# Performance work log

Measured on AMD Instinct MI355X. Metric: run time of the kernel, lower is better.

Reference implementation:

```python
import jax, jax.numpy as jnp
import numpy as np

GAMMA = 0.3      # LinearSpike surrogate slope (Bellec et al. 2018)
TIMESTEPS = 8
DROPOUT = 0.2

@jax.custom_vjp
def spike_fn(mem_thr):
    # forward: Heaviside spike; backward: piecewise-linear surrogate
    return (mem_thr > 0).astype(mem_thr.dtype)

def _spike_fwd(m):
    return (m > 0).astype(m.dtype), m

def _spike_bwd(m, g):
    return (GAMMA * jnp.maximum(1.0 - jnp.abs(m), 0.0) * g,)

spike_fn.defvjp(_spike_fwd, _spike_bwd)

def conv(x, w, stride=1, pad=1):
    return jax.lax.conv_general_dilated(
        x, w, (stride, stride), [(pad, pad), (pad, pad)],
        dimension_numbers=('NCHW', 'OIHW', 'NCHW'))

def avgpool2(x):
    B, C, H, W = x.shape
    return x.reshape(B, C, H // 2, 2, W // 2, 2).mean(axis=(3, 5))

def lif(mem, delta, leak, thr):
    mem = leak * mem + delta                  # leaky integrate
    mem_thr = mem / thr - 1.0                 # normalized membrane
    out = spike_fn(mem_thr)                   # binary spike
    mem = mem - thr * (mem_thr > 0).astype(mem.dtype)  # soft reset
    return mem, out

def setup_inputs() -> dict:
    key = jax.random.key(0)
    ks = jax.random.split(key, 24)
    B = 32
    def w(k, o, i, kh):
        std = float(np.sqrt(2.0 / (kh * kh * o)))  # matches _initialize_weights2
        return jax.random.normal(k, (o, i, kh, kh), jnp.float32) * std
    def mask(k, shape):
        keep = jax.random.bernoulli(k, 1.0 - DROPOUT, shape)
        return keep.astype(jnp.float32) / (1.0 - DROPOUT)
    return {
        'x': jax.random.normal(ks[0], (B, 3, 32, 32), jnp.float32),
        'w_pre0': w(ks[1], 64, 3, 3),
        'w_pre1': w(ks[2], 64, 64, 3),
        'w_pre2': w(ks[3], 64, 64, 3),
        'w1a': w(ks[4], 64, 64, 3),  'w1b': w(ks[5], 64, 64, 3),
        'w2a': w(ks[6], 128, 64, 3), 'w2b': w(ks[7], 128, 128, 3), 'w2i': w(ks[8], 128, 64, 1),
        'w3a': w(ks[9], 256, 128, 3), 'w3b': w(ks[10], 256, 256, 3), 'w3i': w(ks[11], 256, 128, 1),
        'w4a': w(ks[12], 512, 256, 3), 'w4b': w(ks[13], 512, 512, 3), 'w4i': w(ks[14], 512, 256, 1),
        'w_fc': jax.random.normal(ks[15], (10, 512 * 2 * 2), jnp.float32) * 0.01,
        'thr': jnp.ones((11,), jnp.float32),
        'leak': jnp.ones((11,), jnp.float32),
        'mask2': mask(ks[16], (B, 64, 32, 32)),
        'mask5': mask(ks[17], (B, 64, 32, 32)),
        'mask9': mask(ks[18], (B, 64, 16, 16)),
        'mask11': mask(ks[19], (B, 128, 8, 8)),
        'mask13': mask(ks[20], (B, 256, 4, 4)),
        'mask15': mask(ks[21], (B, 512, 2, 2)),
    }

def _forward(x, w_pre0, w_pre1, w_pre2, w1a, w1b, w2a, w2b, w2i,
             w3a, w3b, w3i, w4a, w4b, w4i, w_fc, thr, leak,
             mask2, mask5, mask9, mask11, mask13, mask15):
    B = x.shape[0]
    f32 = jnp.float32
    mems0 = (
        jnp.zeros((B, 64, 32, 32), f32), jnp.zeros((B, 64, 32, 32), f32),
        jnp.zeros((B, 64, 32, 32), f32),
        jnp.zeros((B, 64, 16, 16), f32), jnp.zeros((B, 64, 16, 16), f32),
        jnp.zeros((B, 128, 8, 8), f32), jnp.zeros((B, 128, 8, 8), f32),
        jnp.zeros((B, 256, 4, 4), f32), jnp.zeros((B, 256, 4, 4), f32),
        jnp.zeros((B, 512, 2, 2), f32), jnp.zeros((B, 512, 2, 2), f32),
        jnp.zeros((B, 10), f32),  # output accumulator mem
    )

    def step(carry, _):
        m0, m1, m2, m3, m4, m5, m6, m7, m8, m9, m10, mfc = carry
        # pre_process: (conv->spike->dropout) x2, conv->spike, avgpool2
        m0, o = lif(m0, conv(x, w_pre0), leak[0], thr[0]); o = o * mask2
        m1, o = lif(m1, conv(o, w_pre1), leak[1], thr[1]); o = o * mask5
        m2, o = lif(m2, conv(o, w_pre2), leak[2], thr[2])
        o = avgpool2(o)  # 32x32 -> 16x16
        # layer1 BasicBlock (stride 1, identity shortcut)
        inp = o
        m3, o = lif(m3, conv(inp, w1a), leak[3], thr[3]); o = o * mask9
        m4, o = lif(m4, conv(o, w1b) + inp, leak[4], thr[4])
        # layer2 BasicBlock (stride 2, 1x1 conv shortcut)
        inp = o
        m5, o = lif(m5, conv(inp, w2a, stride=2), leak[5], thr[5]); o = o * mask11
        m6, o = lif(m6, conv(o, w2b) + conv(inp, w2i, stride=2, pad=0), leak[6], thr[6])
        # layer3
        inp = o
        m7, o = lif(m7, conv(inp, w3a, stride=2), leak[7], thr[7]); o = o * mask13
        m8, o = lif(m8, conv(o, w3b) + conv(inp, w3i, stride=2, pad=0), leak[8], thr[8])
        # layer4
        inp = o
        m9, o = lif(m9, conv(inp, w4a, stride=2), leak[9], thr[9]); o = o * mask15
        m10, o = lif(m10, conv(o, w4b) + conv(inp, w4i, stride=2, pad=0), leak[10], thr[10])
        # output layer: pure accumulation of classifier current over timesteps
        mfc = mfc + o.reshape(B, -1) @ w_fc.T
        return (m0, m1, m2, m3, m4, m5, m6, m7, m8, m9, m10, mfc), None

    carry, _ = jax.lax.scan(step, mems0, None, length=TIMESTEPS)
    return carry[-1]  # [B, labels]

def reference(x, w_pre0, w_pre1, w_pre2, w1a, w1b, w2a, w2b, w2i,
              w3a, w3b, w3i, w4a, w4b, w4i, w_fc, thr, leak,
              mask2, mask5, mask9, mask11, mask13, mask15):
    return _forward(x, w_pre0, w_pre1, w_pre2, w1a, w1b, w2a, w2b, w2i,
                    w3a, w3b, w3i, w4a, w4b, w4i, w_fc, thr, leak,
                    mask2, mask5, mask9, mask11, mask13, mask15)
```

## Files before the change

kernel.cpp:

```cpp
#include <hip/hip_runtime.h>

#define BATCH 32

__device__ __forceinline__ float4 ld4(const float* p) { return *(const float4*)p; }

template<int H, int KS>
__global__ __launch_bounds__(256) void conv64_v2(
    const float* __restrict__ in, const float* __restrict__ w,
    float* __restrict__ pbuf)
{
    constexpr int W    = H;
    constexpr int QR   = W / 4;
    constexpr int ROWS = 64 / QR;
    constexpr int RS   = W + 4;
    constexpr int CCT  = 64 / KS;
    constexpr int CC   = (CCT < 8) ? CCT : 8;
    constexpr int NCH  = CCT / CC;
    constexpr int PLANE = (ROWS + 2) * RS;
    constexpr int NTOT = 32 * 64 * H * W;
    constexpr int LCNT = CC * (ROWS + 2) * (W + 2);
    static_assert(NCH == 1 || NCH == 2, "pipeline supports <=2 chunks");
    __shared__ float sIn[CC * PLANE];

    const int tid  = threadIdx.x;
    const int b    = blockIdx.x;
    const int rt   = blockIdx.y;
    const int zc   = blockIdx.z;
    const int cg   = zc & 1;
    const int ks   = zc >> 1;
    const int lane = tid & 63;
    const int g    = __builtin_amdgcn_readfirstlane(tid >> 6);
    const int octet = cg * 32 + g * 8;
    const int r    = lane / QR;
    const int wq   = lane % QR;
    const int ho   = rt * ROWS + r;
    const int row0 = rt * ROWS;

    float acc[8][4] = {};
    const size_t in_b = (size_t)b * 64 * H * W;

    auto stage_val = [&](int i, int c0, float& v) -> int {
        int c   = i / ((ROWS + 2) * (W + 2));
        int rr  = (i / (W + 2)) % (ROWS + 2);
        int col = i % (W + 2);
        int ih  = row0 + rr - 1;
        int iw  = col - 1;
        v = 0.f;
        if ((unsigned)ih < (unsigned)H && (unsigned)iw < (unsigned)W)
            v = in[in_b + (size_t)(c0 + c) * H * W + ih * W + iw];
        return c * PLANE + rr * RS + col;
    };

    auto compute_chunk = [&](int c0) {
        for (int c = 0; c < CC; ++c) {
            float rv[3][6];
            #pragma unroll
            for (int dr = 0; dr < 3; ++dr) {
                const float* p = &sIn[c * PLANE + (r + dr) * RS + wq * 4];
                float4 a  = ld4(p);
                float2 b2 = *(const float2*)(p + 4);
                rv[dr][0] = a.x;  rv[dr][1] = a.y; rv[dr][2] = a.z; rv[dr][3] = a.w;
                rv[dr][4] = b2.x; rv[dr][5] = b2.y;
            }
            const float* wc = w + ((size_t)octet * 64 + (c0 + c)) * 9;
            #pragma unroll
            for (int j = 0; j < 8; ++j) {
                const float* wk = wc + (size_t)j * 64 * 9;
                float w0 = wk[0], w1 = wk[1], w2 = wk[2];
                float w3 = wk[3], w4 = wk[4], w5 = wk[5];
                float w6 = wk[6], w7 = wk[7], w8 = wk[8];
                #pragma unroll
                for (int k = 0; k < 4; ++k) {
                    acc[j][k] = fmaf(rv[0][k + 0], w0, acc[j][k]);
                    acc[j][k] = fmaf(rv[0][k + 1], w1, acc[j][k]);
                    acc[j][k] = fmaf(rv[0][k + 2], w2, acc[j][k]);
                    acc[j][k] = fmaf(rv[1][k + 0], w3, acc[j][k]);
                    acc[j][k] = fmaf(rv[1][k + 1], w4, acc[j][k]);
                    acc[j][k] = fmaf(rv[1][k + 2], w5, acc[j][k]);
                    acc[j][k] = fmaf(rv[2][k + 0], w6, acc[j][k]);
                    acc[j][k] = fmaf(rv[2][k + 1], w7, acc[j][k]);
                    acc[j][k] = fmaf(rv[2][k + 2], w8, acc[j][k]);
                }
            }
        }
    };

    if constexpr (NCH == 1) {
        for (int i = tid; i < LCNT; i += 256) {
            float v; int o = stage_val(i, ks * CCT, v); sIn[o] = v;
        }
        __syncthreads();
        compute_chunk(ks * CCT);
    } else {
        for (int i = tid; i < LCNT; i += 256) {
            float v; int o = stage_val(i, ks * CCT, v); sIn[o] = v;
        }
        constexpr int PF = (LCNT + 255) / 256;
        float pf[PF]; int po[PF];
        #pragma unroll
        for (int k = 0; k < PF; ++k) {
            int i = tid + k * 256; pf[k] = 0.f; po[k] = -1;
            if (i < LCNT) po[k] = stage_val(i, ks * CCT + CC, pf[k]);
        }
        __syncthreads();
        compute_chunk(ks * CCT);
        __syncthreads();
        #pragma unroll
        for (int k = 0; k < PF; ++k) if (po[k] >= 0) sIn[po[k]] = pf[k];
        __syncthreads();
        compute_chunk(ks * CCT + CC);
    }

    #pragma unroll
    for (int j = 0; j < 8; ++j) {
        const size_t idx = ((size_t)(b * 64 + octet + j) * H + ho) * W + wq * 4;
        *(float4*)&pbuf[(size_t)ks * NTOT + idx] =
            make_float4(acc[j][0], acc[j][1], acc[j][2], acc[j][3]);
    }
}

template<int CI, int CO, int KS, int RT>
__global__ __launch_bounds__(256) void conv_mid(
    const float* __restrict__ in, const float* __restrict__ w,
    float* __restrict__ pbuf)
{
    constexpr int HIN = 16, HOUT = 8;
    constexpr int CC  = CI / KS;
    constexpr int NR  = (RT - 1) * 2 + 3;
    constexpr int BSTR = NR * HIN + 4;
    constexpr int CST  = 32 * BSTR;
    constexpr int NTOT = 32 * CO * HOUT * HOUT;
    __shared__ float sBuf[CC * CST];

    const int tid  = threadIdx.x;
    const int lane = tid & 63;
    const int b    = lane >> 1;
    const int ks   = blockIdx.x;
    const int co_u = __builtin_amdgcn_readfirstlane(blockIdx.y * 4 + (tid >> 6));
    const int r0   = blockIdx.z * RT;
    const int g0   = r0 * 2 - 1;

    for (int i = tid; i < CC * 32 * NR * 4; i += 256) {
        int q  = i % 4;
        int s  = (i / 4) % NR;
        int bb = (i / (4 * NR)) % 32;
        int c  = i / (4 * NR * 32);
        int gr = g0 + s;
        float4 v = make_float4(0.f, 0.f, 0.f, 0.f);
        if ((unsigned)gr < (unsigned)HIN)
            v = ld4(&in[(((size_t)bb * CI + ks * CC + c) * HIN + gr) * HIN + q * 4]);
        *(float4*)&sBuf[c * CST + bb * BSTR + s * HIN + q * 4] = v;
    }
    __syncthreads();

    float acc[RT * 8] = {};
    #pragma unroll
    for (int c = 0; c < CC; ++c) {
        const float* wk = w + ((size_t)co_u * CI + ks * CC + c) * 9;
        float wr[9];
        #pragma unroll
        for (int q = 0; q < 9; ++q) wr[q] = wk[q];
        float pl[NR * HIN];
        #pragma unroll
        for (int k = 0; k < NR * 4; ++k) {
            float4 v = ld4(&sBuf[c * CST + b * BSTR + k * 4]);
            pl[k * 4 + 0] = v.x; pl[k * 4 + 1] = v.y;
            pl[k * 4 + 2] = v.z; pl[k * 4 + 3] = v.w;
        }
        #pragma unroll
        for (int j = 0; j < RT; ++j) {
            #pragma unroll
            for (int ow = 0; ow < 8; ++ow) {
                #pragma unroll
                for (int kh = 0; kh < 3; ++kh) {
                    const int s = 2 * j + kh;
                    #pragma unroll
                    for (int kw = 0; kw < 3; ++kw) {
                        const int iw = 2 * ow - 1 + kw;
                        if (iw < 0 || iw >= HIN) continue;
                        acc[j * 8 + ow] = fmaf(pl[s * HIN + iw], wr[kh * 3 + kw],
                                               acc[j * 8 + ow]);
                    }
                }
            }
        }
    }

    if ((lane & 1) == 0) {
        #pragma unroll
        for (int j = 0; j < RT; ++j) {
            const size_t idx = ((size_t)(b * CO + co_u) * HOUT + r0 + j) * HOUT;
            *(float4*)&pbuf[(size_t)ks * NTOT + idx] =
                make_float4(acc[j * 8 + 0], acc[j * 8 + 1], acc[j * 8 + 2], acc[j * 8 + 3]);
            *(float4*)&pbuf[(size_t)ks * NTOT + idx + 4] =
                make_float4(acc[j * 8 + 4], acc[j * 8 + 5], acc[j * 8 + 6], acc[j * 8 + 7]);
        }
    }
}

template<int KS>
__global__ __launch_bounds__(256) void conv_l2b(
    const float* __restrict__ in,
    const float* __restrict__ w,
    const float* __restrict__ sc_in,
    const float* __restrict__ sc_w,
    float* __restrict__ pbuf)
{
    constexpr int CI = 128, CO = 128, SC_CI = 64;
    constexpr int CC  = CI / KS;
    constexpr int SCC = SC_CI / KS;
    constexpr int BSTR = 52, CST = 32 * BSTR;
    constexpr int BSTRs = 36, CSTs = 32 * BSTRs;
    constexpr int NTOT = 32 * CO * 64;
    __shared__ float sBuf[CC * CST];

    const int tid  = threadIdx.x;
    const int lane = tid & 63;
    const int b    = lane >> 1;
    const int co_u = __builtin_amdgcn_readfirstlane(blockIdx.y * 4 + (tid >> 6));
    const int ks   = blockIdx.x;
    const int r0   = blockIdx.z * 4;

    for (int i = tid; i < CC * 32 * 12; i += 256) {
        int f4  = i % 2;
        int row = (i / 2) % 6;
        int bb  = (i / 12) % 32;
        int c   = i / 384;
        int gr  = r0 - 1 + row;
        float4 v = make_float4(0.f, 0.f, 0.f, 0.f);
        if ((unsigned)gr < 8u)
            v = ld4(&in[(((size_t)bb * CI + ks * CC + c) * 8 + gr) * 8 + f4 * 4]);
        *(float4*)&sBuf[c * CST + bb * BSTR + row * 8 + f4 * 4] = v;
    }
    __syncthreads();

    float acc[32] = {};
    #pragma unroll 2
    for (int c = 0; c < CC; ++c) {
        const float* wk = w + ((size_t)co_u * CI + ks * CC + c) * 9;
        float wr[9];
        #pragma unroll
        for (int q = 0; q < 9; ++q) wr[q] = wk[q];
        float pl[48];
        #pragma unroll
        for (int k = 0; k < 12; ++k) {
            float4 v = ld4(&sBuf[c * CST + b * BSTR + k * 4]);
            pl[k * 4 + 0] = v.x; pl[k * 4 + 1] = v.y;
            pl[k * 4 + 2] = v.z; pl[k * 4 + 3] = v.w;
        }
        #pragma unroll
        for (int oh = 0; oh < 4; ++oh) {
            #pragma unroll
            for (int ow = 0; ow < 8; ++ow) {
                #pragma unroll
                for (int kh = 0; kh < 3; ++kh) {
                    #pragma unroll
                    for (int kw = 0; kw < 3; ++kw) {
                        const int iw = ow - 1 + kw;
                        if (iw < 0 || iw >= 8) continue;
                        acc[oh * 8 + ow] = fmaf(pl[(oh + kh) * 8 + iw],
                                                wr[kh * 3 + kw], acc[oh * 8 + ow]);
                    }
                }
            }
        }
    }
    __syncthreads();

    for (int i = tid; i < SCC * 32 * 16; i += 256) {
        int q   = i % 4;
        int row = (i / 4) % 4;
        int bb  = (i / 16) % 32;
        int c   = i / 512;
        float4 v = ld4(&sc_in[
            (((size_t)bb * SC_CI + ks * SCC + c) * 16 + 2 * (r0 + row)) * 16 + q * 4]);
        sBuf[c * CSTs + bb * BSTRs + row * 8 + q * 2 + 0] = v.x;
        sBuf[c * CSTs + bb * BSTRs + row * 8 + q * 2 + 1] = v.z;
    }
    __syncthreads();

    #pragma unroll
    for (int c = 0; c < SCC; ++c) {
        float sw = sc_w[(size_t)co_u * SC_CI + ks * SCC + c];
        #pragma unroll
        for (int p4 = 0; p4 < 8; ++p4) {
            float4 v = ld4(&sBuf[c * CSTs + b * BSTRs + p4 * 4]);
            acc[p4 * 4 + 0] = fmaf(v.x, sw, acc[p4 * 4 + 0]);
            acc[p4 * 4 + 1] = fmaf(v.y, sw, acc[p4 * 4 + 1]);
            acc[p4 * 4 + 2] = fmaf(v.z, sw, acc[p4 * 4 + 2]);
            acc[p4 * 4 + 3] = fmaf(v.w, sw, acc[p4 * 4 + 3]);
        }
    }

    if ((lane & 1) == 0) {
        #pragma unroll
        for (int oh = 0; oh < 4; ++oh) {
            const size_t idx = ((size_t)(b * CO + co_u) * 8 + r0 + oh) * 8;
            *(float4*)&pbuf[(size_t)ks * NTOT + idx]     =
                make_float4(acc[oh * 8 + 0], acc[oh * 8 + 1], acc[oh * 8 + 2], acc[oh * 8 + 3]);
            *(float4*)&pbuf[(size_t)ks * NTOT + idx + 4] =
                make_float4(acc[oh * 8 + 4], acc[oh * 8 + 5], acc[oh * 8 + 6], acc[oh * 8 + 7]);
        }
    }
}

template<int CI, int HIN, int STRIDE, int CO, int SC_CI, int SC_HIN,
         int KS, int COB>
__global__ __launch_bounds__(COB * 64) void conv_ks(
    const float* __restrict__ in, const float* __restrict__ w,
    const float* __restrict__ sc_in, const float* __restrict__ sc_w,
    float* __restrict__ pbuf)
{
    constexpr int NT   = COB * 64;
    constexpr int HOUT = (STRIDE == 2) ? HIN / 2 : HIN;
    constexpr int P    = HOUT * HOUT;
    constexpr int NPIX = HIN * HIN;
    constexpr int CC   = CI / KS;
    constexpr int SCC  = (SC_CI > 0) ? SC_CI / KS : 0;
    constexpr int BSTR = NPIX + (((NPIX / 4) % 2 == 0) ? 4 : 0);
    constexpr int CST  = 32 * BSTR;
    constexpr int BSTRs = P + (((P / 4) % 2 == 0) ? 4 : 0);
    constexpr int CSTs  = 32 * BSTRs;
    static_assert(CI % KS == 0, "ks split");
    static_assert(NPIX % 4 == 0 && P % 4 == 0, "vector widths");

    __shared__ float sIn[CC * CST];
    __shared__ float sSc[(SCC > 0) ? SCC * CSTs : 1];

    const int tid  = threadIdx.x;
    const int lane = tid & 63;
    const int b    = lane >> 1;
    const int ks   = blockIdx.x;
    const int co_u = __builtin_amdgcn_readfirstlane(blockIdx.y * COB + (tid >> 6));
    const int cb   = ks * CC;

    constexpr int NF4 = CC * 32 * (NPIX / 4);
    for (int i = tid; i < NF4; i += NT) {
        int k4 = i % (NPIX / 4);
        int c  = (i / (NPIX / 4)) % CC;
        int bb = i / ((NPIX / 4) * CC);
        float4 v = ld4(&in[((size_t)bb * CI + cb + c) * NPIX + k4 * 4]);
        *(float4*)&sIn[c * CST + bb * BSTR + k4 * 4] = v;
    }
    if constexpr (SCC > 0) {
        constexpr int NH  = HOUT / 2;
        constexpr int NSC = SCC * 32 * HOUT * NH;
        for (int i = tid; i < NSC; i += NT) {
            int hc = i % NH;
            int r  = (i / NH) % HOUT;
            int c  = (i / (NH * HOUT)) % SCC;
            int bb = i / (NH * HOUT * SCC);
            float4 v = ld4(&sc_in[
                ((size_t)(bb * SC_CI + ks * SCC + c) * SC_HIN + 2 * r) * SC_HIN
                + hc * 4]);
            sSc[c * CSTs + bb * BSTRs + r * HOUT + hc * 2 + 0] = v.x;
            sSc[c * CSTs + bb * BSTRs + r * HOUT + hc * 2 + 1] = v.z;
        }
    }
    __syncthreads();

    float acc[P] = {};

    const float* wbase = w + ((size_t)co_u * CI + cb) * 9;
    #pragma unroll 4
    for (int j = 0; j < CC; ++j) {
        float wr[9];
        #pragma unroll
        for (int q = 0; q < 9; ++q) wr[q] = wbase[j * 9 + q];
        float plane[NPIX];
        #pragma unroll
        for (int r4 = 0; r4 < NPIX / 4; ++r4) {
            float4 v = ld4(&sIn[j * CST + b * BSTR + r4 * 4]);
            plane[r4 * 4 + 0] = v.x; plane[r4 * 4 + 1] = v.y;
            plane[r4 * 4 + 2] = v.z; plane[r4 * 4 + 3] = v.w;
        }
        #pragma unroll
        for (int ho = 0; ho < HOUT; ++ho) {
            #pragma unroll
            for (int wo = 0; wo < HOUT; ++wo) {
                #pragma unroll
                for (int kh = 0; kh < 3; ++kh) {
                    const int ih = ho * STRIDE - 1 + kh;
                    if (ih < 0 || ih >= HIN) continue;
                    #pragma unroll
                    for (int kw = 0; kw < 3; ++kw) {
                        const int iw = wo * STRIDE - 1 + kw;
                        if (iw < 0 || iw >= HIN) continue;
                        acc[ho * HOUT + wo] =
                            fmaf(plane[ih * HIN + iw], wr[kh * 3 + kw],
                                 acc[ho * HOUT + wo]);
                    }
                }
            }
        }
    }

    if constexpr (SCC > 0) {
        const float* swb = sc_w + (size_t)co_u * SC_CI + ks * SCC;
        #pragma unroll 4
        for (int j = 0; j < SCC; ++j) {
            float sw = swb[j];
            #pragma unroll
            for (int p4 = 0; p4 < P / 4; ++p4) {
                float4 v = ld4(&sSc[j * CSTs + b * BSTRs + p4 * 4]);
                acc[p4 * 4 + 0] = fmaf(v.x, sw, acc[p4 * 4 + 0]);
                acc[p4 * 4 + 1] = fmaf(v.y, sw, acc[p4 * 4 + 1]);
                acc[p4 * 4 + 2] = fmaf(v.z, sw, acc[p4 * 4 + 2]);
                acc[p4 * 4 + 3] = fmaf(v.w, sw, acc[p4 * 4 + 3]);
            }
        }
    }

    if ((lane & 1) == 0) {
        float* pp = pbuf + (((size_t)ks * 32 + b) * CO + co_u) * P;
        #pragma unroll
        for (int p4 = 0; p4 < P / 4; ++p4)
            *(float4*)&pp[p4 * 4] = make_float4(acc[p4 * 4], acc[p4 * 4 + 1],
                                                acc[p4 * 4 + 2], acc[p4 * 4 + 3]);
    }
}

__device__ __forceinline__ void lif_store4(
    float4 s, float* __restrict__ mem, const float* __restrict__ mask,
    float* __restrict__ out, float* __restrict__ accum,
    size_t idx, float thr, float leak)
{
    float4 m4 = ld4(&mem[idx]);
    float4 k4 = mask ? ld4(&mask[idx]) : make_float4(1.f, 1.f, 1.f, 1.f);
    float4 mo, oo;
    float m0 = fmaf(leak, m4.x, s.x); float s0 = (m0 / thr - 1.0f > 0.f) ? 1.f : 0.f;
    mo.x = m0 - thr * s0; oo.x = s0 * k4.x;
    float m1 = fmaf(leak, m4.y, s.y); float s1 = (m1 / thr - 1.0f > 0.f) ? 1.f : 0.f;
    mo.y = m1 - thr * s1; oo.y = s1 * k4.y;
    float m2 = fmaf(leak, m4.z, s.z); float s2 = (m2 / thr - 1.0f > 0.f) ? 1.f : 0.f;
    mo.z = m2 - thr * s2; oo.z = s2 * k4.z;
    float m3 = fmaf(leak, m4.w, s.w); float s3 = (m3 / thr - 1.0f > 0.f) ? 1.f : 0.f;
    mo.w = m3 - thr * s3; oo.w = s3 * k4.w;
    *(float4*)&mem[idx] = mo;
    *(float4*)&out[idx] = oo;
    if (accum) {
        float4 a4 = ld4(&accum[idx]);
        a4.x += oo.x; a4.y += oo.y; a4.z += oo.z; a4.w += oo.w;
        *(float4*)&accum[idx] = a4;
    }
}

template<int CO, int P, int KS>
__global__ __launch_bounds__(256) void reduce_lif(
    const float* __restrict__ pbuf,
    const float* __restrict__ res,
    float* __restrict__ mem,
    const float* __restrict__ thr_a, const float* __restrict__ leak_a, int layer,
    const float* __restrict__ mask, float* __restrict__ out,
    float* __restrict__ accum)
{
    constexpr int TOT4 = 32 * CO * P / 4;
    const int i4 = blockIdx.x * 256 + threadIdx.x;
    if (i4 >= TOT4) return;
    const float4* pb4 = (const float4*)pbuf;
    float4 s = pb4[i4];
    #pragma unroll 4
    for (int ks = 1; ks < KS; ++ks) {
        float4 v = pb4[(size_t)ks * TOT4 + i4];
        s.x += v.x; s.y += v.y; s.z += v.z; s.w += v.w;
    }
    const size_t idx = (size_t)i4 * 4;
    if (res) {
        float4 r4 = ld4(&res[idx]);
        s.x += r4.x; s.y += r4.y; s.z += r4.z; s.w += r4.w;
    }
    lif_store4(s, mem, mask, out, accum, idx, thr_a[layer], leak_a[layer]);
}

template<int KS>
__global__ __launch_bounds__(256) void reduce_lif_pool(
    const float* __restrict__ pbuf, float* __restrict__ mem,
    const float* __restrict__ thr_a, const float* __restrict__ leak_a, int layer,
    float* __restrict__ pool_out)
{
    constexpr int TOT = 32 * 64 * 32 * 32;
    const int i = blockIdx.x * 256 + threadIdx.x;
    const int q  = i % 8;
    const int rp = (i / 8) % 16;
    const int c  = (i / 128) % 64;
    const int b  = i / 8192;
    const size_t idx0 = (((size_t)(b * 64 + c) * 32) + 2 * rp) * 32 + 4 * q;
    const size_t idx1 = idx0 + 32;

    float4 s0 = ld4(&pbuf[idx0]);
    float4 s1 = ld4(&pbuf[idx1]);
    #pragma unroll 4
    for (int ks = 1; ks < KS; ++ks) {
        float4 v0 = ld4(&pbuf[(size_t)ks * TOT + idx0]);
        float4 v1 = ld4(&pbuf[(size_t)ks * TOT + idx1]);
        s0.x += v0.x; s0.y += v0.y; s0.z += v0.z; s0.w += v0.w;
        s1.x += v1.x; s1.y += v1.y; s1.z += v1.z; s1.w += v1.w;
    }
    const float thr  = thr_a[layer];
    const float leak = leak_a[layer];
    float4 m0 = ld4(&mem[idx0]), m1 = ld4(&mem[idx1]);
    float4 n0, n1, o0, o1;
    {
        float m = fmaf(leak, m0.x, s0.x); float sp = (m / thr - 1.0f > 0.f) ? 1.f : 0.f;
        n0.x = m - thr * sp; o0.x = sp;
        m = fmaf(leak, m0.y, s0.y); sp = (m / thr - 1.0f > 0.f) ? 1.f : 0.f;
        n0.y = m - thr * sp; o0.y = sp;
        m = fmaf(leak, m0.z, s0.z); sp = (m / thr - 1.0f > 0.f) ? 1.f : 0.f;
        n0.z = m - thr * sp; o0.z = sp;
        m = fmaf(leak, m0.w, s0.w); sp = (m / thr - 1.0f > 0.f) ? 1.f : 0.f;
        n0.w = m - thr * sp; o0.w = sp;
        m = fmaf(leak, m1.x, s1.x); sp = (m / thr - 1.0f > 0.f) ? 1.f : 0.f;
        n1.x = m - thr * sp; o1.x = sp;
        m = fmaf(leak, m1.y, s1.y); sp = (m / thr - 1.0f > 0.f) ? 1.f : 0.f;
        n1.y = m - thr * sp; o1.y = sp;
        m = fmaf(leak, m1.z, s1.z); sp = (m / thr - 1.0f > 0.f) ? 1.f : 0.f;
        n1.z = m - thr * sp; o1.z = sp;
        m = fmaf(leak, m1.w, s1.w); sp = (m / thr - 1.0f > 0.f) ? 1.f : 0.f;
        n1.w = m - thr * sp; o1.w = sp;
    }
    *(float4*)&mem[idx0] = n0;
    *(float4*)&mem[idx1] = n1;
    float2 pv;
    pv.x = (o0.x + o0.y + o1.x + o1.y) * 0.25f;
    pv.y = (o0.z + o0.w + o1.z + o1.w) * 0.25f;
    *(float2*)&pool_out[(((size_t)(b * 64 + c) * 16) + rp) * 16 + 2 * q] = pv;
}

template<int KS>
__global__ __launch_bounds__(256) void reduce_l4b_lif0(
    const float* __restrict__ pbuf, float* __restrict__ mem10,
    const float* __restrict__ thr_a, const float* __restrict__ leak_a,
    float* __restrict__ out_s2b, float* __restrict__ ssum,
    const float4* __restrict__ delta, float4* __restrict__ mem0,
    const float4* __restrict__ mask, float4* __restrict__ s32a)
{
    if (blockIdx.x < 64) {
        constexpr int TOT4 = 32 * 512;
        const int i4 = blockIdx.x * 256 + threadIdx.x;
        if (i4 >= TOT4) return;
        const float4* pb4 = (const float4*)pbuf;
        float4 s = pb4[i4];
        #pragma unroll 4
        for (int ks = 1; ks < KS; ++ks) {
            float4 v = pb4[(size_t)ks * TOT4 + i4];
            s.x += v.x; s.y += v.y; s.z += v.z; s.w += v.w;
        }
        lif_store4(s, mem10, nullptr, out_s2b, ssum,
                   (size_t)i4 * 4, thr_a[10], leak_a[10]);
    } else {
        const int i = (blockIdx.x - 64) * 256 + threadIdx.x;
        float thr = thr_a[0], leak = leak_a[0];
        float4 d = delta[i], m4 = mem0[i], k4 = mask[i], mo, oo;
        float m0 = fmaf(leak, m4.x, d.x); float s0 = (m0 / thr - 1.0f > 0.f) ? 1.f : 0.f;
        mo.x = m0 - thr * s0; oo.x = s0 * k4.x;
        float m1 = fmaf(leak, m4.y, d.y); float s1 = (m1 / thr - 1.0f > 0.f) ? 1.f : 0.f;
        mo.y = m1 - thr * s1; oo.y = s1 * k4.y;
        float m2 = fmaf(leak, m4.z, d.z); float s2 = (m2 / thr - 1.0f > 0.f) ? 1.f : 0.f;
        mo.z = m2 - thr * s2; oo.z = s2 * k4.z;
        float m3 = fmaf(leak, m4.w, d.w); float s3 = (m3 / thr - 1.0f > 0.f) ? 1.f : 0.f;
        mo.w = m3 - thr * s3; oo.w = s3 * k4.w;
        mem0[i] = mo; s32a[i] = oo;
    }
}

__global__ __launch_bounds__(256) void conv_raw_kernel(
    const float* __restrict__ in, const float* __restrict__ w,
    float* __restrict__ out,
    int Ci, int Co, int Hin, int Win, int total)
{
    int idx = blockIdx.x * blockDim.x + threadIdx.x;
    if (idx >= total) return;
    int wo = idx % Win;
    int t  = idx / Win;
    int ho = t % Hin; t /= Hin;
    int co = t % Co;
    int b  = t / Co;
    int ih0 = ho - 1, iw0 = wo - 1;
    const float* wp = w + (size_t)co * Ci * 9;
    const float* ip = in + (size_t)b * Ci * Hin * Win;
    bool hv0 = (unsigned)(ih0)     < (unsigned)Hin;
    bool hv1 = (unsigned)(ih0 + 1) < (unsigned)Hin;
    bool hv2 = (unsigned)(ih0 + 2) < (unsigned)Hin;
    bool wv0 = (unsigned)(iw0)     < (unsigned)Win;
    bool wv1 = (unsigned)(iw0 + 1) < (unsigned)Win;
    bool wv2 = (unsigned)(iw0 + 2) < (unsigned)Win;
    float acc = 0.f;
    int plane = Hin * Win;
    for (int ci = 0; ci < Ci; ++ci) {
        const float* irow = ip + ci * plane;
        const float* wk   = wp + ci * 9;
        if (hv0) {
            const float* r = irow + ih0 * Win;
            if (wv0) acc = fmaf(r[iw0],     wk[0], acc);
            if (wv1) acc = fmaf(r[iw0 + 1], wk[1], acc);
            if (wv2) acc = fmaf(r[iw0 + 2], wk[2], acc);
        }
        if (hv1) {
            const float* r = irow + (ih0 + 1) * Win;
            if (wv0) acc = fmaf(r[iw0],     wk[3], acc);
            if (wv1) acc = fmaf(r[iw0 + 1], wk[4], acc);
            if (wv2) acc = fmaf(r[iw0 + 2], wk[5], acc);
        }
        if (hv2) {
            const float* r = irow + (ih0 + 2) * Win;
            if (wv0) acc = fmaf(r[iw0],     wk[6], acc);
            if (wv1) acc = fmaf(r[iw0 + 1], wk[7], acc);
            if (wv2) acc = fmaf(r[iw0 + 2], wk[8], acc);
        }
    }
    out[idx] = acc;
}

__global__ __launch_bounds__(256) void lif0_kernel(
    const float4* __restrict__ delta, float4* __restrict__ mem,
    const float* __restrict__ thr_a, const float* __restrict__ leak_a,
    const float4* __restrict__ mask, float4* __restrict__ out, int total4)
{
    int i = blockIdx.x * blockDim.x + threadIdx.x;
    if (i >= total4) return;
    float thr = thr_a[0], leak = leak_a[0];
    float4 d = delta[i], m4 = mem[i], k4 = mask[i], mo, oo;
    float m0 = fmaf(leak, m4.x, d.x); float s0 = (m0 / thr - 1.0f > 0.f) ? 1.f : 0.f;
    mo.x = m0 - thr * s0; oo.x = s0 * k4.x;
    float m1 = fmaf(leak, m4.y, d.y); float s1 = (m1 / thr - 1.0f > 0.f) ? 1.f : 0.f;
    mo.y = m1 - thr * s1; oo.y = s1 * k4.y;
    float m2 = fmaf(leak, m4.z, d.z); float s2 = (m2 / thr - 1.0f > 0.f) ? 1.f : 0.f;
    mo.z = m2 - thr * s2; oo.z = s2 * k4.z;
    float m3 = fmaf(leak, m4.w, d.w); float s3 = (m3 / thr - 1.0f > 0.f) ? 1.f : 0.f;
    mo.w = m3 - thr * s3; oo.w = s3 * k4.w;
    mem[i] = mo; out[i] = oo;
}

__global__ __launch_bounds__(64) void fc_kernel(
    const float* __restrict__ s, const float* __restrict__ wfc,
    float* __restrict__ out)
{
    int bk = blockIdx.x;
    int b = bk / 10, k = bk % 10;
    const float* sp = s   + (size_t)b * 2048;
    const float* wp = wfc + (size_t)k * 2048;
    float acc = 0.f;
    for (int j = threadIdx.x; j < 2048; j += 64)
        acc = fmaf(sp[j], wp[j], acc);
    #pragma unroll
    for (int off = 32; off; off >>= 1)
        acc += __shfl_down(acc, off, 64);
    if (threadIdx.x == 0) out[b * 10 + k] = acc;
}

extern "C" void kernel_launch(void* const* d_in, const int* in_sizes, int n_in,
                              void* d_out, int out_size, void* d_ws, size_t ws_size,
                              hipStream_t stream) {
    const float* x      = (const float*)d_in[0];
    const float* w_pre0 = (const float*)d_in[1];
    const float* w_pre1 = (const float*)d_in[2];
    const float* w_pre2 = (const float*)d_in[3];
    const float* w1a    = (const float*)d_in[4];
    const float* w1b    = (const float*)d_in[5];
    const float* w2a    = (const float*)d_in[6];
    const float* w2b    = (const float*)d_in[7];
    const float* w2i    = (const float*)d_in[8];
    const float* w3a    = (const float*)d_in[9];
    const float* w3b    = (const float*)d_in[10];
    const float* w3i    = (const float*)d_in[11];
    const float* w4a    = (const float*)d_in[12];
    const float* w4b    = (const float*)d_in[13];
    const float* w4i    = (const float*)d_in[14];
    const float* w_fc   = (const float*)d_in[15];
    const float* thr    = (const float*)d_in[16];
    const float* leak   = (const float*)d_in[17];
    const float* mask2  = (const float*)d_in[18];
    const float* mask5  = (const float*)d_in[19];
    const float* mask9  = (const float*)d_in[20];
    const float* mask11 = (const float*)d_in[21];
    const float* mask13 = (const float*)d_in[22];
    const float* mask15 = (const float*)d_in[23];

    float* ws = (float*)d_ws;
    size_t off = 0;
    auto alloc = [&](size_t n) { float* p = ws + off; off += n; return p; };
    float* m0  = alloc(2097152);
    float* m1  = alloc(2097152);
    float* m2  = alloc(2097152);
    float* m3  = alloc(524288);
    float* m4  = alloc(524288);
    float* m5  = alloc(262144);
    float* m6  = alloc(262144);
    float* m7  = alloc(131072);
    float* m8  = alloc(131072);
    float* m9  = alloc(65536);
    float* m10 = alloc(65536);
    float* ssum = alloc(65536);
    size_t zero_floats = off;
    float* delta0  = alloc(2097152);
    float* s32_a   = alloc(2097152);
    float* s32_b   = alloc(2097152);
    float* s16_inp = alloc(524288);
    float* s16_a   = alloc(524288);
    float* s16_b   = alloc(524288);
    float* s8_a    = alloc(262144);
    float* s8_b    = alloc(262144);
    float* s4_a    = alloc(131072);
    float* s4_b    = alloc(131072);
    float* s2_a    = alloc(65536);
    float* s2_b    = alloc(65536);
    float* pbuf    = alloc(16777216);
    (void)ws_size; (void)in_sizes; (void)n_in; (void)out_size;

    hipMemsetAsync(d_ws, 0, zero_floats * sizeof(float), stream);

    auto grid = [](int total) { return dim3((total + 255) / 256); };

    {
        int total = BATCH * 64 * 32 * 32;
        conv_raw_kernel<<<grid(total), 256, 0, stream>>>(
            x, w_pre0, delta0, 3, 64, 32, 32, total);
    }

    int n32 = BATCH * 64 * 32 * 32;
    lif0_kernel<<<grid(n32 / 4), 256, 0, stream>>>(
        (const float4*)delta0, (float4*)m0, thr, leak,
        (const float4*)mask2, (float4*)s32_a, n32 / 4);

    for (int t = 0; t < 8; ++t) {
        conv64_v2<32, 4><<<dim3(BATCH, 4, 8), 256, 0, stream>>>(s32_a, w_pre1, pbuf);
        reduce_lif<64, 1024, 4><<<dim3(2048), 256, 0, stream>>>(
            pbuf, nullptr, m1, thr, leak, 1, mask5, s32_b, nullptr);
        conv64_v2<32, 4><<<dim3(BATCH, 4, 8), 256, 0, stream>>>(s32_b, w_pre2, pbuf);
        reduce_lif_pool<4><<<dim3(1024), 256, 0, stream>>>(
            pbuf, m2, thr, leak, 2, s16_inp);
        conv64_v2<16, 8><<<dim3(BATCH, 1, 16), 256, 0, stream>>>(s16_inp, w1a, pbuf);
        reduce_lif<64, 256, 8><<<dim3(512), 256, 0, stream>>>(
            pbuf, nullptr, m3, thr, leak, 3, mask9, s16_a, nullptr);
        conv64_v2<16, 8><<<dim3(BATCH, 1, 16), 256, 0, stream>>>(s16_a, w1b, pbuf);
        reduce_lif<64, 256, 8><<<dim3(512), 256, 0, stream>>>(
            pbuf, s16_inp, m4, thr, leak, 4, nullptr, s16_b, nullptr);

        conv_mid<64, 128, 32, 2><<<dim3(32, 32, 4), 256, 0, stream>>>(
            s16_b, w2a, pbuf);
        reduce_lif<128, 64, 32><<<dim3(256), 256, 0, stream>>>(
            pbuf, nullptr, m5, thr, leak, 5, mask11, s8_a, nullptr);
        conv_l2b<16><<<dim3(16, 32, 2), 256, 0, stream>>>(
            s8_a, w2b, s16_b, w2i, pbuf);
        reduce_lif<128, 64, 16><<<dim3(256), 256, 0, stream>>>(
            pbuf, nullptr, m6, thr, leak, 6, nullptr, s8_b, nullptr);
        conv_ks<128, 8, 2, 256, 0, 0, 32, 4><<<dim3(32, 64), 256, 0, stream>>>(
            s8_b, w3a, nullptr, nullptr, pbuf);
        reduce_lif<256, 16, 32><<<dim3(128), 256, 0, stream>>>(
            pbuf, nullptr, m7, thr, leak, 7, mask13, s4_a, nullptr);
        conv_ks<256, 4, 1, 256, 128, 8, 16, 4><<<dim3(16, 64), 256, 0, stream>>>(
            s4_a, w3b, s8_b, w3i, pbuf);
        reduce_lif<256, 16, 16><<<dim3(128), 256, 0, stream>>>(
            pbuf, nullptr, m8, thr, leak, 8, nullptr, s4_b, nullptr);
        conv_ks<256, 4, 2, 512, 0, 0, 16, 4><<<dim3(16, 128), 256, 0, stream>>>(
            s4_b, w4a, nullptr, nullptr, pbuf);
        reduce_lif<512, 4, 16><<<dim3(64), 256, 0, stream>>>(
            pbuf, nullptr, m9, thr, leak, 9, mask15, s2_a, nullptr);
        conv_ks<512, 2, 1, 512, 256, 4, 16, 4><<<dim3(16, 128), 256, 0, stream>>>(
            s2_a, w4b, s4_b, w4i, pbuf);
        if (t < 7) {
            reduce_l4b_lif0<16><<<dim3(64 + 2048), 256, 0, stream>>>(
                pbuf, m10, thr, leak, s2_b, ssum,
                (const float4*)delta0, (float4*)m0, (const float4*)mask2,
                (float4*)s32_a);
        } else {
            reduce_lif<512, 4, 16><<<dim3(64), 256, 0, stream>>>(
                pbuf, nullptr, m10, thr, leak, 10, nullptr, s2_b, ssum);
        }
    }

    fc_kernel<<<dim3(320), dim3(64), 0, stream>>>(ssum, w_fc, (float*)d_out);
}
```

Before: 2.755 ms.

## Halve conv64 block size to cut register pressure, prefetch shortcut input in conv_l2b

The conv64_v2 kernels now run 128-thread blocks, with each block covering 16 output channels instead of 32 and the grid z dimension doubled. The prefetch no longer keeps per-element shared-memory offsets in registers; offsets are recomputed when storing. This lowers register use and adds blocks, but every block now stages the input tile for only half as many channels, which doubles redundant global loads. Separately, conv_l2b issues its shortcut-input global loads before the main 3x3 compute so their latency overlaps with the math, at the cost of extra registers.

```diff
diff --git a/kernel.cpp b/kernel.cpp
--- a/kernel.cpp
+++ b/kernel.cpp
@@ -5,7 +5,7 @@
 __device__ __forceinline__ float4 ld4(const float* p) { return *(const float4*)p; }
 
 template<int H, int KS>
-__global__ __launch_bounds__(256) void conv64_v2(
+__global__ __launch_bounds__(128) void conv64_v2(
     const float* __restrict__ in, const float* __restrict__ w,
     float* __restrict__ pbuf)
 {
@@ -19,6 +19,7 @@
     constexpr int PLANE = (ROWS + 2) * RS;
     constexpr int NTOT = 32 * 64 * H * W;
     constexpr int LCNT = CC * (ROWS + 2) * (W + 2);
+    constexpr int NT   = 128;
     static_assert(NCH == 1 || NCH == 2, "pipeline supports <=2 chunks");
     __shared__ float sIn[CC * PLANE];
 
@@ -26,11 +27,11 @@
     const int b    = blockIdx.x;
     const int rt   = blockIdx.y;
     const int zc   = blockIdx.z;
-    const int cg   = zc & 1;
-    const int ks   = zc >> 1;
+    const int cg   = zc & 3;
+    const int ks   = zc >> 2;
     const int lane = tid & 63;
     const int g    = __builtin_amdgcn_readfirstlane(tid >> 6);
-    const int octet = cg * 32 + g * 8;
+    const int octet = cg * 16 + g * 8;
     const int r    = lane / QR;
     const int wq   = lane % QR;
     const int ho   = rt * ROWS + r;
@@ -39,16 +40,22 @@
     float acc[8][4] = {};
     const size_t in_b = (size_t)b * 64 * H * W;
 
-    auto stage_val = [&](int i, int c0, float& v) -> int {
+    auto stage_off = [&](int i) -> int {
+        int c   = i / ((ROWS + 2) * (W + 2));
+        int rr  = (i / (W + 2)) % (ROWS + 2);
+        int col = i % (W + 2);
+        return c * PLANE + rr * RS + col;
+    };
+    auto stage_val = [&](int i, int c0) -> float {
         int c   = i / ((ROWS + 2) * (W + 2));
         int rr  = (i / (W + 2)) % (ROWS + 2);
         int col = i % (W + 2);
         int ih  = row0 + rr - 1;
         int iw  = col - 1;
-        v = 0.f;
+        float v = 0.f;
         if ((unsigned)ih < (unsigned)H && (unsigned)iw < (unsigned)W)
             v = in[in_b + (size_t)(c0 + c) * H * W + ih * W + iw];
-        return c * PLANE + rr * RS + col;
+        return v;
     };
 
     auto compute_chunk = [&](int c0) {
@@ -86,27 +93,28 @@
     };
 
     if constexpr (NCH == 1) {
-        for (int i = tid; i < LCNT; i += 256) {
-            float v; int o = stage_val(i, ks * CCT, v); sIn[o] = v;
-        }
+        for (int i = tid; i < LCNT; i += NT)
+            sIn[stage_off(i)] = stage_val(i, ks * CCT);
         __syncthreads();
         compute_chunk(ks * CCT);
     } else {
-        for (int i = tid; i < LCNT; i += 256) {
-            float v; int o = stage_val(i, ks * CCT, v); sIn[o] = v;
-        }
-        constexpr int PF = (LCNT + 255) / 256;
-        float pf[PF]; int po[PF];
+        for (int i = tid; i < LCNT; i += NT)
+            sIn[stage_off(i)] = stage_val(i, ks * CCT);
+        constexpr int PF = (LCNT + NT - 1) / NT;
+        float pf[PF];
         #pragma unroll
         for (int k = 0; k < PF; ++k) {
-            int i = tid + k * 256; pf[k] = 0.f; po[k] = -1;
-            if (i < LCNT) po[k] = stage_val(i, ks * CCT + CC, pf[k]);
+            int i = tid + k * NT;
+            pf[k] = (i < LCNT) ? stage_val(i, ks * CCT + CC) : 0.f;
         }
         __syncthreads();
         compute_chunk(ks * CCT);
         __syncthreads();
         #pragma unroll
-        for (int k = 0; k < PF; ++k) if (po[k] >= 0) sIn[po[k]] = pf[k];
+        for (int k = 0; k < PF; ++k) {
+            int i = tid + k * NT;
+            if (i < LCNT) sIn[stage_off(i)] = pf[k];
+        }
         __syncthreads();
         compute_chunk(ks * CCT + CC);
     }
@@ -212,6 +220,8 @@
     constexpr int BSTR = 52, CST = 32 * BSTR;
     constexpr int BSTRs = 36, CSTs = 32 * BSTRs;
     constexpr int NTOT = 32 * CO * 64;
+    constexpr int NSC  = SCC * 32 * 16;
+    constexpr int PFS  = (NSC + 255) / 256;
     __shared__ float sBuf[CC * CST];
 
     const int tid  = threadIdx.x;
@@ -231,6 +241,17 @@
         if ((unsigned)gr < 8u)
             v = ld4(&in[(((size_t)bb * CI + ks * CC + c) * 8 + gr) * 8 + f4 * 4]);
         *(float4*)&sBuf[c * CST + bb * BSTR + row * 8 + f4 * 4] = v;
+    }
+    float4 scpf[PFS];
+    #pragma unroll
+    for (int k = 0; k < PFS; ++k) {
+        int i = tid + k * 256;
+        int q   = i % 4;
+        int row = (i / 4) % 4;
+        int bb  = (i / 16) % 32;
+        int c   = i / 512;
+        scpf[k] = ld4(&sc_in[
+            (((size_t)bb * SC_CI + ks * SCC + c) * 16 + 2 * (r0 + row)) * 16 + q * 4]);
     }
     __syncthreads();
 
@@ -267,15 +288,15 @@
     }
     __syncthreads();
 
-    for (int i = tid; i < SCC * 32 * 16; i += 256) {
+    #pragma unroll
+    for (int k = 0; k < PFS; ++k) {
+        int i = tid + k * 256;
         int q   = i % 4;
         int row = (i / 4) % 4;
         int bb  = (i / 16) % 32;
         int c   = i / 512;
-        float4 v = ld4(&sc_in[
-            (((size_t)bb * SC_CI + ks * SCC + c) * 16 + 2 * (r0 + row)) * 16 + q * 4]);
-        sBuf[c * CSTs + bb * BSTRs + row * 8 + q * 2 + 0] = v.x;
-        sBuf[c * CSTs + bb * BSTRs + row * 8 + q * 2 + 1] = v.z;
+        sBuf[c * CSTs + bb * BSTRs + row * 8 + q * 2 + 0] = scpf[k].x;
+        sBuf[c * CSTs + bb * BSTRs + row * 8 + q * 2 + 1] = scpf[k].z;
     }
     __syncthreads();
 
@@ -723,16 +744,16 @@
         (const float4*)mask2, (float4*)s32_a, n32 / 4);
 
     for (int t = 0; t < 8; ++t) {
-        conv64_v2<32, 4><<<dim3(BATCH, 4, 8), 256, 0, stream>>>(s32_a, w_pre1, pbuf);
+        conv64_v2<32, 4><<<dim3(BATCH, 4, 16), 128, 0, stream>>>(s32_a, w_pre1, pbuf);
         reduce_lif<64, 1024, 4><<<dim3(2048), 256, 0, stream>>>(
             pbuf, nullptr, m1, thr, leak, 1, mask5, s32_b, nullptr);
-        conv64_v2<32, 4><<<dim3(BATCH, 4, 8), 256, 0, stream>>>(s32_b, w_pre2, pbuf);
+        conv64_v2<32, 4><<<dim3(BATCH, 4, 16), 128, 0, stream>>>(s32_b, w_pre2, pbuf);
         reduce_lif_pool<4><<<dim3(1024), 256, 0, stream>>>(
             pbuf, m2, thr, leak, 2, s16_inp);
-        conv64_v2<16, 8><<<dim3(BATCH, 1, 16), 256, 0, stream>>>(s16_inp, w1a, pbuf);
+        conv64_v2<16, 8><<<dim3(BATCH, 1, 32), 128, 0, stream>>>(s16_inp, w1a, pbuf);
         reduce_lif<64, 256, 8><<<dim3(512), 256, 0, stream>>>(
             pbuf, nullptr, m3, thr, leak, 3, mask9, s16_a, nullptr);
-        conv64_v2<16, 8><<<dim3(BATCH, 1, 16), 256, 0, stream>>>(s16_a, w1b, pbuf);
+        conv64_v2<16, 8><<<dim3(BATCH, 1, 32), 128, 0, stream>>>(s16_a, w1b, pbuf);
         reduce_lif<64, 256, 8><<<dim3(512), 256, 0, stream>>>(
             pbuf, s16_inp, m4, thr, leak, 4, nullptr, s16_b, nullptr);
 
```

After: 3.010 ms. 9.2% more time.
